# Performance work log

Measured on AMD Instinct MI355X. Metric: run time of the kernel, lower is better.

Reference implementation:

```python
import jax, jax.numpy as jnp
import numpy as np

K = 2  # num_experts_used (top-k)


def setup_inputs() -> dict:
    key = jax.random.key(0)
    ks = jax.random.split(key, 6)
    B, S, D, U, E = 2, 2048, 1024, 4096, 8
    return {
        "x": jax.random.normal(ks[0], (B, S, D), dtype=jnp.float32),
        "w_router": jax.random.normal(ks[1], (E, D), dtype=jnp.float32),
        "w_up": jax.random.normal(ks[2], (E, U, D), dtype=jnp.float32),
        "b_up": jax.random.normal(ks[3], (E, U), dtype=jnp.float32),
        "w_down": jax.random.normal(ks[4], (E, D, U), dtype=jnp.float32),
        "b_down": jax.random.normal(ks[5], (E, D), dtype=jnp.float32),
    }


def reference(x, w_router, w_up, b_up, w_down, b_down):
    # Router: Linear(embed_dim -> num_experts), no bias
    logits = jnp.einsum('bsd,ed->bse', x, w_router)
    top_logits, idx = jax.lax.top_k(logits, K)          # [b,s,k]
    router_weights = jax.nn.softmax(top_logits, axis=-1)  # softmax over top-k logits

    # Compute all-expert FFN outputs (same math as per-token gathered weights,
    # without materializing the (b,s,k,u,d) weight copies of the original).
    h = jnp.einsum('eud,bsd->bseu', w_up, x) + b_up[None, None]   # [b,s,E,u]
    h = jax.nn.gelu(h, approximate=False)
    y = jnp.einsum('edu,bseu->bsed', w_down, h) + b_down[None, None]  # [b,s,E,d]

    # Gather outputs of the top-k experts per token
    y_k = jnp.take_along_axis(y, idx[..., None], axis=2)  # [b,s,k,d]
    out = jnp.einsum('bskd,bsk->bsd', y_k, router_weights)
    return out
```

## Files before the change

kernel.cpp:

```cpp
#include <hip/hip_runtime.h>
#include <hip/hip_bf16.h>
#include <stdint.h>
#include <math.h>

#define TTOK 4096
#define DDIM 1024
#define UDIM 4096
#define NEXP 8
#define KSPLIT 2
#define KCH   (UDIM / KSPLIT)
#define NPAIR (TTOK * 2)
#define EPAD 72
#define CPAD 32
#define RBLK 128
#define CBLK 2048

using float4v = __attribute__((ext_vector_type(4))) float;
using short8  = __attribute__((ext_vector_type(8))) short;
using ushort8 = __attribute__((ext_vector_type(8))) unsigned short;
using ushort4v = __attribute__((ext_vector_type(4))) unsigned short;

__device__ __forceinline__ unsigned short f2bf(float f) {
  union { float f; unsigned u; } v; v.f = f;
  unsigned r = v.u + 0x7FFFu + ((v.u >> 16) & 1u);
  return (unsigned short)(r >> 16);
}
__device__ __forceinline__ float bf2f(unsigned short u) {
  union { unsigned u; float f; } v; v.u = ((unsigned)u) << 16;
  return v.f;
}
__device__ __forceinline__ void load_lds16(const void* g, void* l) {
  __builtin_amdgcn_global_load_lds(
      (const __attribute__((address_space(1))) unsigned int*)g,
      (__attribute__((address_space(3))) unsigned int*)l, 16, 0, 0);
}
__device__ __forceinline__ short8 cvt8(const float4v a, const float4v b) {
  union { __hip_bfloat162 h[4]; short8 s; } u;
  u.h[0] = __float22bfloat162_rn(make_float2(a[0], a[1]));
  u.h[1] = __float22bfloat162_rn(make_float2(a[2], a[3]));
  u.h[2] = __float22bfloat162_rn(make_float2(b[0], b[1]));
  u.h[3] = __float22bfloat162_rn(make_float2(b[2], b[3]));
  return u.s;
}
__device__ __forceinline__ float gelu_f(float v) {
  float u = v * (0.7978845608f + 0.0356774081f * v * v);
  float ex = __expf(2.0f * u);
  return v * (1.0f - 1.0f / (1.0f + ex));
}

__global__ void router_kernel(const float* __restrict__ x,
                              const float* __restrict__ wr,
                              int* __restrict__ counts, int* __restrict__ list,
                              float* __restrict__ wpair, int* __restrict__ epair,
                              unsigned short* __restrict__ xb) {
  const int t = blockIdx.x * 4 + (threadIdx.x >> 6);
  const int lane = threadIdx.x & 63;
  float acc[NEXP];
#pragma unroll
  for (int e = 0; e < NEXP; e++) acc[e] = 0.0f;
  const float* xr = x + (size_t)t * DDIM;
  unsigned short* xbr = xb + (size_t)t * DDIM;
  for (int d = lane; d < DDIM; d += 64) {
    float xv = xr[d];
    xbr[d] = f2bf(xv);
#pragma unroll
    for (int e = 0; e < NEXP; e++) acc[e] += xv * wr[e * DDIM + d];
  }
#pragma unroll
  for (int e = 0; e < NEXP; e++) {
#pragma unroll
    for (int off = 32; off > 0; off >>= 1) acc[e] += __shfl_xor(acc[e], off, 64);
  }
  if (lane == 0) {
    int e0 = 0; float l0 = acc[0];
    for (int e = 1; e < NEXP; e++) if (acc[e] > l0) { l0 = acc[e]; e0 = e; }
    int e1 = -1; float l1 = -3.4e38f;
    for (int e = 0; e < NEXP; e++) if (e != e0 && acc[e] > l1) { l1 = acc[e]; e1 = e; }
    float s1 = expf(l1 - l0);
    float inv = 1.0f / (1.0f + s1);
    int p0 = atomicAdd(&counts[e0 * CPAD], 1);
    list[e0 * TTOK + p0] = 2 * t;
    wpair[2 * t] = inv;  epair[2 * t] = e0;
    int p1 = atomicAdd(&counts[e1 * CPAD], 1);
    list[e1 * TTOK + p1] = 2 * t + 1;
    wpair[2 * t + 1] = s1 * inv;  epair[2 * t + 1] = e1;
  }
}

__global__ void prep_kernel(const float* __restrict__ x, const float* __restrict__ wr,
                            int* __restrict__ counts, int* __restrict__ list,
                            float* __restrict__ wpair, int* __restrict__ epair,
                            unsigned short* __restrict__ xb,
                            const float* __restrict__ wu, const float* __restrict__ wd,
                            unsigned short* __restrict__ wub, unsigned short* __restrict__ wdb) {
  __shared__ int sE0[32], sE1[32];
  const int bid = blockIdx.x;
  const int tid = threadIdx.x;

  if (bid < RBLK) {
    const int wave = tid >> 6, lane = tid & 63;
#pragma unroll 1
    for (int j = 0; j < 8; j++) {
      const int slot = wave * 8 + j;
      const int t = bid * 32 + slot;
      float acc[NEXP];
#pragma unroll
      for (int e = 0; e < NEXP; e++) acc[e] = 0.0f;
      const float* xr = x + (size_t)t * DDIM;
      unsigned short* xbr = xb + (size_t)t * DDIM;
#pragma unroll
      for (int it = 0; it < 4; it++) {
        const int d = it * 256 + lane * 4;
        float4v xv = *(const float4v*)(xr + d);
        ushort4v xo;
#pragma unroll
        for (int c = 0; c < 4; c++) xo[c] = f2bf(xv[c]);
        *(ushort4v*)(xbr + d) = xo;
#pragma unroll
        for (int e = 0; e < NEXP; e++) {
          float4v wv = *(const float4v*)(wr + e * DDIM + d);
          acc[e] += xv[0] * wv[0] + xv[1] * wv[1] + xv[2] * wv[2] + xv[3] * wv[3];
        }
      }
#pragma unroll
      for (int e = 0; e < NEXP; e++) {
#pragma unroll
        for (int off = 32; off > 0; off >>= 1) acc[e] += __shfl_xor(acc[e], off, 64);
      }
      if (lane == 0) {
        int e0 = 0; float l0 = acc[0];
        for (int e = 1; e < NEXP; e++) if (acc[e] > l0) { l0 = acc[e]; e0 = e; }
        int e1 = -1; float l1 = -3.4e38f;
        for (int e = 0; e < NEXP; e++) if (e != e0 && acc[e] > l1) { l1 = acc[e]; e1 = e; }
        float s1 = expf(l1 - l0);
        float inv = 1.0f / (1.0f + s1);
        wpair[2 * t] = inv;          epair[2 * t] = e0;
        wpair[2 * t + 1] = s1 * inv; epair[2 * t + 1] = e1;
        sE0[slot] = e0;  sE1[slot] = e1;
      }
    }
    __syncthreads();
    if (tid < NEXP) {
      const int e = tid;
      int cnt = 0;
#pragma unroll
      for (int s = 0; s < 32; s++) cnt += (sE0[s] == e) + (sE1[s] == e);
      int r = atomicAdd(&counts[e * CPAD], cnt);
      int* le = list + e * TTOK;
#pragma unroll 1
      for (int s = 0; s < 32; s++) {
        const int p = 2 * (bid * 32 + s);
        if (sE0[s] == e) le[r++] = p;
        if (sE1[s] == e) le[r++] = p + 1;
      }
    }
    return;
  }

  const int cb = bid - RBLK;
  const float* s; unsigned short* d;
  size_t i0;
  if (cb < CBLK / 2) { s = wu; d = wub; i0 = (size_t)cb * 4096; }
  else               { s = wd; d = wdb; i0 = (size_t)(cb - CBLK / 2) * 4096; }
#pragma unroll
  for (int it = 0; it < 16; it++) {
    const size_t i = i0 + (size_t)it * 256 + tid;
    float4v lo = *(const float4v*)(s + i * 8);
    float4v hi = *(const float4v*)(s + i * 8 + 4);
    *(short8*)(d + i * 8) = cvt8(lo, hi);
  }
}

__global__ __launch_bounds__(256, 4) void stage_up_b16(
    const unsigned short* __restrict__ xb, const unsigned short* __restrict__ wub,
    const float* __restrict__ bup, const int* __restrict__ counts,
    const int* __restrict__ list, unsigned short* __restrict__ h) {
  const int e = blockIdx.z, mt = blockIdx.y, nt = blockIdx.x;
  const int cnt = counts[e * CPAD];
  if (mt * 128 >= cnt) return;
  const int rem = min(128, cnt - mt * 128);
  const int* lst = list + e * TTOK + mt * 128;

  __shared__ __align__(16) char SM[18432];
  unsigned short* Sb = (unsigned short*)SM;

  const int tid = threadIdx.x;
  const int wave = tid >> 6, lane = tid & 63;
  const int srow = tid >> 2, cell = tid & 3;

  const int tok0 = lst[min(srow, rem - 1)] >> 1;
  const int tok1 = lst[min(srow + 64, rem - 1)] >> 1;
  const unsigned short* a0 = xb + (size_t)tok0 * DDIM + cell * 8;
  const unsigned short* a1 = xb + (size_t)tok1 * DDIM + cell * 8;
  const unsigned short* b0 = wub + ((size_t)e * UDIM + nt * 128 + srow) * DDIM + cell * 8;
  const unsigned short* b1 = b0 + (size_t)64 * DDIM;

  const int wm = wave >> 1, wn = wave & 1;
  const int lane15 = lane & 15, quad = lane >> 4;
  const int abyte = (wm * 64 + lane15) * 64 + quad * 16;
  const int bbyte = 8192 + (wn * 64 + lane15) * 64 + quad * 16;

  float4v acc[4][4];
#pragma unroll
  for (int i = 0; i < 4; i++)
#pragma unroll
    for (int j = 0; j < 4; j++) acc[i][j] = (float4v){0.f, 0.f, 0.f, 0.f};

  for (int k0 = 0; k0 < DDIM; k0 += 32) {
    load_lds16(a0 + k0, SM + tid * 16);
    load_lds16(a1 + k0, SM + 4096 + tid * 16);
    load_lds16(b0 + k0, SM + 8192 + tid * 16);
    load_lds16(b1 + k0, SM + 12288 + tid * 16);
    __syncthreads();
    short8 af[4], bfr[4];
#pragma unroll
    for (int mi = 0; mi < 4; mi++) af[mi] = *(const short8*)(SM + abyte + mi * 1024);
#pragma unroll
    for (int ni = 0; ni < 4; ni++) bfr[ni] = *(const short8*)(SM + bbyte + ni * 1024);
#pragma unroll
    for (int mi = 0; mi < 4; mi++)
#pragma unroll
      for (int ni = 0; ni < 4; ni++)
        acc[mi][ni] = __builtin_amdgcn_mfma_f32_16x16x32_bf16(af[mi], bfr[ni], acc[mi][ni], 0, 0, 0);
    __syncthreads();
  }

  const int ucol0 = nt * 128 + wn * 64;
  float bias[4];
#pragma unroll
  for (int ni = 0; ni < 4; ni++) bias[ni] = bup[e * UDIM + ucol0 + ni * 16 + lane15];
  const int row = tid >> 1, seg = tid & 1;
  const int opair = (row < rem) ? lst[row] : -1;
#pragma unroll
  for (int hh = 0; hh < 2; hh++) {
    if (wn == hh) {
#pragma unroll
      for (int mi = 0; mi < 4; mi++)
#pragma unroll
        for (int r = 0; r < 4; r++) {
          const int rl = wm * 64 + mi * 16 + quad * 4 + r;
#pragma unroll
          for (int ni = 0; ni < 4; ni++)
            Sb[rl * EPAD + ni * 16 + lane15] = f2bf(gelu_f(acc[mi][ni][r] + bias[ni]));
        }
    }
    __syncthreads();
    if (opair >= 0) {
      unsigned short* dst = h + (size_t)opair * UDIM + nt * 128 + hh * 64 + seg * 32;
      const unsigned short* src = Sb + row * EPAD + seg * 32;
#pragma unroll
      for (int c = 0; c < 4; c++) *(ushort8*)(dst + c * 8) = *(const ushort8*)(src + c * 8);
    }
    __syncthreads();
  }
}

__global__ __launch_bounds__(256, 4) void stage_down_b16(
    const unsigned short* __restrict__ h, const unsigned short* __restrict__ wdb,
    const int* __restrict__ counts, const int* __restrict__ list,
    unsigned short* __restrict__ part) {
  const int e = blockIdx.z, mt = blockIdx.y >> 1, kc = blockIdx.y & 1, nt = blockIdx.x;
  const int cnt = counts[e * CPAD];
  if (mt * 128 >= cnt) return;
  const int rem = min(128, cnt - mt * 128);
  const int* lst = list + e * TTOK + mt * 128;

  __shared__ __align__(16) char SM[18432];
  unsigned short* Sb = (unsigned short*)SM;

  const int tid = threadIdx.x;
  const int wave = tid >> 6, lane = tid & 63;
  const int srow = tid >> 2, cell = tid & 3;

  const int pr0 = lst[min(srow, rem - 1)];
  const int pr1 = lst[min(srow + 64, rem - 1)];
  const unsigned short* a0 = h + (size_t)pr0 * UDIM + kc * KCH + cell * 8;
  const unsigned short* a1 = h + (size_t)pr1 * UDIM + kc * KCH + cell * 8;
  const unsigned short* b0 = wdb + ((size_t)e * DDIM + nt * 128 + srow) * UDIM + kc * KCH + cell * 8;
  const unsigned short* b1 = b0 + (size_t)64 * UDIM;

  const int wm = wave >> 1, wn = wave & 1;
  const int lane15 = lane & 15, quad = lane >> 4;
  const int abyte = (wm * 64 + lane15) * 64 + quad * 16;
  const int bbyte = 8192 + (wn * 64 + lane15) * 64 + quad * 16;

  float4v acc[4][4];
#pragma unroll
  for (int i = 0; i < 4; i++)
#pragma unroll
    for (int j = 0; j < 4; j++) acc[i][j] = (float4v){0.f, 0.f, 0.f, 0.f};

  for (int k0 = 0; k0 < KCH; k0 += 32) {
    load_lds16(a0 + k0, SM + tid * 16);
    load_lds16(a1 + k0, SM + 4096 + tid * 16);
    load_lds16(b0 + k0, SM + 8192 + tid * 16);
    load_lds16(b1 + k0, SM + 12288 + tid * 16);
    __syncthreads();
    short8 af[4], bfr[4];
#pragma unroll
    for (int mi = 0; mi < 4; mi++) af[mi] = *(const short8*)(SM + abyte + mi * 1024);
#pragma unroll
    for (int ni = 0; ni < 4; ni++) bfr[ni] = *(const short8*)(SM + bbyte + ni * 1024);
#pragma unroll
    for (int mi = 0; mi < 4; mi++)
#pragma unroll
      for (int ni = 0; ni < 4; ni++)
        acc[mi][ni] = __builtin_amdgcn_mfma_f32_16x16x32_bf16(af[mi], bfr[ni], acc[mi][ni], 0, 0, 0);
    __syncthreads();
  }

  const int row = tid >> 1, seg = tid & 1;
  const int opair = (row < rem) ? lst[row] : -1;
#pragma unroll
  for (int hh = 0; hh < 2; hh++) {
    if (wn == hh) {
#pragma unroll
      for (int mi = 0; mi < 4; mi++)
#pragma unroll
        for (int r = 0; r < 4; r++) {
          const int rl = wm * 64 + mi * 16 + quad * 4 + r;
#pragma unroll
          for (int ni = 0; ni < 4; ni++)
            Sb[rl * EPAD + ni * 16 + lane15] = f2bf(acc[mi][ni][r]);
        }
    }
    __syncthreads();
    if (opair >= 0) {
      unsigned short* dst = part + ((size_t)kc * NPAIR + opair) * DDIM + nt * 128 + hh * 64 + seg * 32;
      const unsigned short* src = Sb + row * EPAD + seg * 32;
#pragma unroll
      for (int c = 0; c < 4; c++) *(ushort8*)(dst + c * 8) = *(const ushort8*)(src + c * 8);
    }
    __syncthreads();
  }
}

__global__ __launch_bounds__(256, 3) void stage_up_k(
    const unsigned short* __restrict__ xb, const float* __restrict__ wu,
    const float* __restrict__ bup, const int* __restrict__ counts,
    const int* __restrict__ list, unsigned short* __restrict__ h) {
  const int e = blockIdx.z, mt = blockIdx.y, nt = blockIdx.x;
  const int cnt = counts[e * CPAD];
  if (mt * 128 >= cnt) return;
  const int rem = min(128, cnt - mt * 128);
  const int* lst = list + e * TTOK + mt * 128;

  __shared__ __align__(16) char SM[24576];
  unsigned short* Sb = (unsigned short*)SM;

  const int tid = threadIdx.x;
  const int wave = tid >> 6, lane = tid & 63;
  const int srow = tid >> 2, cell = tid & 3;
  const int brow = tid >> 3;
  const int bswz = (tid & 7) ^ (brow & 7);

  const int tok0 = lst[min(srow, rem - 1)] >> 1;
  const int tok1 = lst[min(srow + 64, rem - 1)] >> 1;
  const unsigned short* a0 = xb + (size_t)tok0 * DDIM + cell * 8;
  const unsigned short* a1 = xb + (size_t)tok1 * DDIM + cell * 8;
  const float* bbase = wu + ((size_t)e * UDIM + nt * 128) * DDIM;
  const float* bsrc[4];
#pragma unroll
  for (int k = 0; k < 4; k++) bsrc[k] = bbase + (size_t)(brow + k * 32) * DDIM + bswz * 4;

  const int wm = wave >> 1, wn = wave & 1;
  const int lane15 = lane & 15, quad = lane >> 4;
  const int abyte = (wm * 64 + lane15) * 64 + quad * 16;
  const int p0 = (2 * quad) ^ (lane & 7);
  const int bbyte = 8192 + (wn * 64 + lane15) * 128;

  float4v acc[4][4];
#pragma unroll
  for (int i = 0; i < 4; i++)
#pragma unroll
    for (int j = 0; j < 4; j++) acc[i][j] = (float4v){0.f, 0.f, 0.f, 0.f};

  for (int k0 = 0; k0 < DDIM; k0 += 32) {
    load_lds16(a0 + k0, SM + tid * 16);
    load_lds16(a1 + k0, SM + 4096 + tid * 16);
#pragma unroll
    for (int k = 0; k < 4; k++) load_lds16(bsrc[k] + k0, SM + 8192 + k * 4096 + tid * 16);
    __syncthreads();
    short8 af[4], bfr[4];
#pragma unroll
    for (int mi = 0; mi < 4; mi++) af[mi] = *(const short8*)(SM + abyte + mi * 1024);
#pragma unroll
    for (int ni = 0; ni < 4; ni++) {
      const char* rb = SM + bbyte + ni * 2048;
      float4v f0 = *(const float4v*)(rb + p0 * 16);
      float4v f1 = *(const float4v*)(rb + (p0 ^ 1) * 16);
      bfr[ni] = cvt8(f0, f1);
    }
#pragma unroll
    for (int mi = 0; mi < 4; mi++)
#pragma unroll
      for (int ni = 0; ni < 4; ni++)
        acc[mi][ni] = __builtin_amdgcn_mfma_f32_16x16x32_bf16(af[mi], bfr[ni], acc[mi][ni], 0, 0, 0);
    __syncthreads();
  }

  const int ucol0 = nt * 128 + wn * 64;
  float bias[4];
#pragma unroll
  for (int ni = 0; ni < 4; ni++) bias[ni] = bup[e * UDIM + ucol0 + ni * 16 + lane15];
  const int row = tid >> 1, seg = tid & 1;
  const int opair = (row < rem) ? lst[row] : -1;
#pragma unroll
  for (int hh = 0; hh < 2; hh++) {
    if (wn == hh) {
#pragma unroll
      for (int mi = 0; mi < 4; mi++)
#pragma unroll
        for (int r = 0; r < 4; r++) {
          const int rl = wm * 64 + mi * 16 + quad * 4 + r;
#pragma unroll
          for (int ni = 0; ni < 4; ni++)
            Sb[rl * EPAD + ni * 16 + lane15] = f2bf(gelu_f(acc[mi][ni][r] + bias[ni]));
        }
    }
    __syncthreads();
    if (opair >= 0) {
      unsigned short* dst = h + (size_t)opair * UDIM + nt * 128 + hh * 64 + seg * 32;
      const unsigned short* src = Sb + row * EPAD + seg * 32;
#pragma unroll
      for (int c = 0; c < 4; c++) *(ushort8*)(dst + c * 8) = *(const ushort8*)(src + c * 8);
    }
    __syncthreads();
  }
}

template <bool PARTM>
__global__ __launch_bounds__(256, 3) void stage_down_k(
    const unsigned short* __restrict__ h, const float* __restrict__ wd,
    const float* __restrict__ bdn, const float* __restrict__ wpair,
    const int* __restrict__ counts, const int* __restrict__ list,
    unsigned short* __restrict__ part, float* __restrict__ out) {
  const int e = blockIdx.z, mt = blockIdx.y >> 1, kc = blockIdx.y & 1, nt = blockIdx.x;
  const int cnt = counts[e * CPAD];
  if (mt * 128 >= cnt) return;
  const int rem = min(128, cnt - mt * 128);
  const int* lst = list + e * TTOK + mt * 128;

  __shared__ __align__(16) char SM[24576];
  unsigned short* Sb = (unsigned short*)SM;

  const int tid = threadIdx.x;
  const int wave = tid >> 6, lane = tid & 63;
  const int srow = tid >> 2, cell = tid & 3;
  const int brow = tid >> 3;
  const int bswz = (tid & 7) ^ (brow & 7);

  const int pr0 = lst[min(srow, rem - 1)];
  const int pr1 = lst[min(srow + 64, rem - 1)];
  const unsigned short* a0 = h + (size_t)pr0 * UDIM + kc * KCH + cell * 8;
  const unsigned short* a1 = h + (size_t)pr1 * UDIM + kc * KCH + cell * 8;
  const float* bbase = wd + ((size_t)e * DDIM + nt * 128) * UDIM + kc * KCH;
  const float* bsrc[4];
#pragma unroll
  for (int k = 0; k < 4; k++) bsrc[k] = bbase + (size_t)(brow + k * 32) * UDIM + bswz * 4;

  const int wm = wave >> 1, wn = wave & 1;
  const int lane15 = lane & 15, quad = lane >> 4;
  const int abyte = (wm * 64 + lane15) * 64 + quad * 16;
  const int p0 = (2 * quad) ^ (lane & 7);
  const int bbyte = 8192 + (wn * 64 + lane15) * 128;

  float4v acc[4][4];
#pragma unroll
  for (int i = 0; i < 4; i++)
#pragma unroll
    for (int j = 0; j < 4; j++) acc[i][j] = (float4v){0.f, 0.f, 0.f, 0.f};

  for (int k0 = 0; k0 < KCH; k0 += 32) {
    load_lds16(a0 + k0, SM + tid * 16);
    load_lds16(a1 + k0, SM + 4096 + tid * 16);
#pragma unroll
    for (int k = 0; k < 4; k++) load_lds16(bsrc[k] + k0, SM + 8192 + k * 4096 + tid * 16);
    __syncthreads();
    short8 af[4], bfr[4];
#pragma unroll
    for (int mi = 0; mi < 4; mi++) af[mi] = *(const short8*)(SM + abyte + mi * 1024);
#pragma unroll
    for (int ni = 0; ni < 4; ni++) {
      const char* rb = SM + bbyte + ni * 2048;
      float4v f0 = *(const float4v*)(rb + p0 * 16);
      float4v f1 = *(const float4v*)(rb + (p0 ^ 1) * 16);
      bfr[ni] = cvt8(f0, f1);
    }
#pragma unroll
    for (int mi = 0; mi < 4; mi++)
#pragma unroll
      for (int ni = 0; ni < 4; ni++)
        acc[mi][ni] = __builtin_amdgcn_mfma_f32_16x16x32_bf16(af[mi], bfr[ni], acc[mi][ni], 0, 0, 0);
    __syncthreads();
  }

  const int dcol0 = nt * 128 + wn * 64;
  if constexpr (PARTM) {
    const int row = tid >> 1, seg = tid & 1;
    const int opair = (row < rem) ? lst[row] : -1;
#pragma unroll
    for (int hh = 0; hh < 2; hh++) {
      if (wn == hh) {
#pragma unroll
        for (int mi = 0; mi < 4; mi++)
#pragma unroll
          for (int r = 0; r < 4; r++) {
            const int rl = wm * 64 + mi * 16 + quad * 4 + r;
#pragma unroll
            for (int ni = 0; ni < 4; ni++)
              Sb[rl * EPAD + ni * 16 + lane15] = f2bf(acc[mi][ni][r]);
          }
      }
      __syncthreads();
      if (opair >= 0) {
        unsigned short* dst = part + ((size_t)kc * NPAIR + opair) * DDIM + nt * 128 + hh * 64 + seg * 32;
        const unsigned short* src = Sb + row * EPAD + seg * 32;
#pragma unroll
        for (int c = 0; c < 4; c++) *(ushort8*)(dst + c * 8) = *(const ushort8*)(src + c * 8);
      }
      __syncthreads();
    }
  } else {
    float bias[4];
#pragma unroll
    for (int ni = 0; ni < 4; ni++)
      bias[ni] = (kc == 0) ? bdn[e * DDIM + dcol0 + ni * 16 + lane15] : 0.0f;
#pragma unroll
    for (int mi = 0; mi < 4; mi++)
#pragma unroll
      for (int r = 0; r < 4; r++) {
        const int mrow = wm * 64 + mi * 16 + quad * 4 + r;
        if (mrow < rem) {
          const int pair = lst[mrow];
          const float w = wpair[pair];
          float* orow = out + (size_t)(pair >> 1) * DDIM;
#pragma unroll
          for (int ni = 0; ni < 4; ni++)
            atomicAdd(&orow[dcol0 + ni * 16 + lane15], w * (acc[mi][ni][r] + bias[ni]));
        }
      }
  }
}

__global__ void combine_kernel(const unsigned short* __restrict__ part,
                               const float* __restrict__ bdn,
                               const float* __restrict__ wpair,
                               const int* __restrict__ epair,
                               float* __restrict__ out) {
  const int idx = blockIdx.x * 256 + threadIdx.x;
  const int t = idx >> 7, c8 = (idx & 127) * 8;
  const size_t kstride = (size_t)NPAIR * DDIM;
  const unsigned short* pa = part + (size_t)(2 * t) * DDIM + c8;
  float s0[8], s1[8];
#pragma unroll
  for (int j = 0; j < 8; j++) { s0[j] = 0.f; s1[j] = 0.f; }
#pragma unroll
  for (int kc = 0; kc < KSPLIT; kc++) {
    ushort8 a = *(const ushort8*)(pa + kc * kstride);
    ushort8 b = *(const ushort8*)(pa + kc * kstride + DDIM);
#pragma unroll
    for (int j = 0; j < 8; j++) { s0[j] += bf2f(a[j]); s1[j] += bf2f(b[j]); }
  }
  const float w0 = wpair[2 * t], w1 = wpair[2 * t + 1];
  const int e0 = epair[2 * t], e1 = epair[2 * t + 1];
  const float* b0 = bdn + e0 * DDIM + c8;
  const float* b1 = bdn + e1 * DDIM + c8;
  float4v o[2];
#pragma unroll
  for (int half = 0; half < 2; half++)
#pragma unroll
    for (int j = 0; j < 4; j++) {
      const int jj = half * 4 + j;
      o[half][j] = w0 * (s0[jj] + b0[jj]) + w1 * (s1[jj] + b1[jj]);
    }
  float4v* dst = (float4v*)(out + (size_t)t * DDIM + c8);
  dst[0] = o[0]; dst[1] = o[1];
}

__global__ void zero_out_k(float4v* __restrict__ out) {
  const int tid = blockIdx.x * blockDim.x + threadIdx.x;
  const int O4 = TTOK * DDIM / 4;
  const int stride = gridDim.x * blockDim.x;
  for (int i = tid; i < O4; i += stride) out[i] = (float4v){0.f, 0.f, 0.f, 0.f};
}

extern "C" void kernel_launch(void* const* d_in, const int* in_sizes, int n_in,
                              void* d_out, int out_size, void* d_ws, size_t ws_size,
                              hipStream_t stream) {
  (void)in_sizes; (void)n_in; (void)out_size;
  const float* x        = (const float*)d_in[0];
  const float* w_router = (const float*)d_in[1];
  const float* w_up     = (const float*)d_in[2];
  const float* b_up     = (const float*)d_in[3];
  const float* w_down   = (const float*)d_in[4];
  const float* b_down   = (const float*)d_in[5];
  float* out = (float*)d_out;

  char* ws = (char*)d_ws;
  size_t off = 0;
  auto take = [&](size_t b) { size_t o = off; off = (off + b + 255) & ~(size_t)255; return o; };
  unsigned short* h  = (unsigned short*)(ws + take((size_t)NPAIR * UDIM * 2));
  unsigned short* xb = (unsigned short*)(ws + take((size_t)TTOK * DDIM * 2));
  int* counts        = (int*)(ws + take(NEXP * CPAD * 4));
  int* list          = (int*)(ws + take((size_t)NEXP * TTOK * 4));
  float* wpair       = (float*)(ws + take((size_t)NPAIR * 4));
  int* epair         = (int*)(ws + take((size_t)NPAIR * 4));
  size_t part_off    = take((size_t)KSPLIT * NPAIR * DDIM * 2);
  const bool partmode = ws_size >= off;
  size_t wub_off     = take((size_t)NEXP * UDIM * DDIM * 2);
  size_t wdb_off     = take((size_t)NEXP * DDIM * UDIM * 2);
  const bool bf16mode = ws_size >= off;

  hipMemsetAsync(counts, 0, NEXP * CPAD * 4, stream);

  if (bf16mode) {
    unsigned short* part = (unsigned short*)(ws + part_off);
    unsigned short* wub  = (unsigned short*)(ws + wub_off);
    unsigned short* wdb  = (unsigned short*)(ws + wdb_off);
    prep_kernel<<<RBLK + CBLK, 256, 0, stream>>>(
        x, w_router, counts, list, wpair, epair, xb, w_up, w_down, wub, wdb);
    stage_up_b16<<<dim3(UDIM / 128, 32, NEXP), 256, 0, stream>>>(
        xb, wub, b_up, counts, list, h);
    stage_down_b16<<<dim3(DDIM / 128, 32 * KSPLIT, NEXP), 256, 0, stream>>>(
        h, wdb, counts, list, part);
    combine_kernel<<<TTOK * DDIM / 8 / 256, 256, 0, stream>>>(part, b_down, wpair, epair, out);
  } else {
    router_kernel<<<TTOK / 4, 256, 0, stream>>>(x, w_router, counts, list, wpair, epair, xb);
    stage_up_k<<<dim3(UDIM / 128, 32, NEXP), 256, 0, stream>>>(xb, w_up, b_up, counts, list, h);
    if (partmode) {
      unsigned short* part = (unsigned short*)(ws + part_off);
      stage_down_k<true><<<dim3(DDIM / 128, 32 * KSPLIT, NEXP), 256, 0, stream>>>(
          h, w_down, b_down, wpair, counts, list, part, out);
      combine_kernel<<<TTOK * DDIM / 8 / 256, 256, 0, stream>>>(part, b_down, wpair, epair, out);
    } else {
      zero_out_k<<<1024, 256, 0, stream>>>((float4v*)out);
      stage_down_k<false><<<dim3(DDIM / 128, 32 * KSPLIT, NEXP), 256, 0, stream>>>(
          h, w_down, b_down, wpair, counts, list, (unsigned short*)nullptr, out);
    }
  }
}
```

Measured before the change: 602.9 us.

## Reorder prep blocks, use nontemporal weight conversion, expert-major grids, rework fallback path

```diff
diff --git a/kernel.cpp b/kernel.cpp
--- a/kernel.cpp
+++ b/kernel.cpp
@@ -14,6 +14,7 @@
 #define CPAD 32
 #define RBLK 128
 #define CBLK 2048
+#define RTOK 16
 
 using float4v = __attribute__((ext_vector_type(4))) float;
 using short8  = __attribute__((ext_vector_type(8))) short;
@@ -33,6 +34,12 @@
   __builtin_amdgcn_global_load_lds(
       (const __attribute__((address_space(1))) unsigned int*)g,
       (__attribute__((address_space(3))) unsigned int*)l, 16, 0, 0);
+}
+__device__ __forceinline__ float4v ntld4(const float* p) {
+  return __builtin_nontemporal_load((const float4v*)p);
+}
+__device__ __forceinline__ void ntst8(unsigned short* p, const short8 v) {
+  __builtin_nontemporal_store(v, (short8*)p);
 }
 __device__ __forceinline__ short8 cvt8(const float4v a, const float4v b) {
   union { __hip_bfloat162 h[4]; short8 s; } u;
@@ -46,45 +53,6 @@
   float u = v * (0.7978845608f + 0.0356774081f * v * v);
   float ex = __expf(2.0f * u);
   return v * (1.0f - 1.0f / (1.0f + ex));
-}
-
-__global__ void router_kernel(const float* __restrict__ x,
-                              const float* __restrict__ wr,
-                              int* __restrict__ counts, int* __restrict__ list,
-                              float* __restrict__ wpair, int* __restrict__ epair,
-                              unsigned short* __restrict__ xb) {
-  const int t = blockIdx.x * 4 + (threadIdx.x >> 6);
-  const int lane = threadIdx.x & 63;
-  float acc[NEXP];
-#pragma unroll
-  for (int e = 0; e < NEXP; e++) acc[e] = 0.0f;
-  const float* xr = x + (size_t)t * DDIM;
-  unsigned short* xbr = xb + (size_t)t * DDIM;
-  for (int d = lane; d < DDIM; d += 64) {
-    float xv = xr[d];
-    xbr[d] = f2bf(xv);
-#pragma unroll
-    for (int e = 0; e < NEXP; e++) acc[e] += xv * wr[e * DDIM + d];
-  }
-#pragma unroll
-  for (int e = 0; e < NEXP; e++) {
-#pragma unroll
-    for (int off = 32; off > 0; off >>= 1) acc[e] += __shfl_xor(acc[e], off, 64);
-  }
-  if (lane == 0) {
-    int e0 = 0; float l0 = acc[0];
-    for (int e = 1; e < NEXP; e++) if (acc[e] > l0) { l0 = acc[e]; e0 = e; }
-    int e1 = -1; float l1 = -3.4e38f;
-    for (int e = 0; e < NEXP; e++) if (e != e0 && acc[e] > l1) { l1 = acc[e]; e1 = e; }
-    float s1 = expf(l1 - l0);
-    float inv = 1.0f / (1.0f + s1);
-    int p0 = atomicAdd(&counts[e0 * CPAD], 1);
-    list[e0 * TTOK + p0] = 2 * t;
-    wpair[2 * t] = inv;  epair[2 * t] = e0;
-    int p1 = atomicAdd(&counts[e1 * CPAD], 1);
-    list[e1 * TTOK + p1] = 2 * t + 1;
-    wpair[2 * t + 1] = s1 * inv;  epair[2 * t + 1] = e1;
-  }
 }
 
 __global__ void prep_kernel(const float* __restrict__ x, const float* __restrict__ wr,
@@ -97,77 +65,81 @@
   const int bid = blockIdx.x;
   const int tid = threadIdx.x;
 
-  if (bid < RBLK) {
-    const int wave = tid >> 6, lane = tid & 63;
+  if (bid < CBLK) {
+    const float* s; unsigned short* d; size_t i0;
+    if (bid < CBLK / 2) { s = wu; d = wub; i0 = (size_t)bid * 4096; }
+    else                { s = wd; d = wdb; i0 = (size_t)(bid - CBLK / 2) * 4096; }
+    const float* sp = s + (i0 + tid) * 8;
+    unsigned short* dp = d + (i0 + tid) * 8;
+    float4v p0 = ntld4(sp), p1 = ntld4(sp + 4);
+#pragma unroll
+    for (int it = 0; it < 16; it++) {
+      float4v c0 = p0, c1 = p1;
+      if (it + 1 < 16) {
+        p0 = ntld4(sp + (size_t)(it + 1) * 2048);
+        p1 = ntld4(sp + (size_t)(it + 1) * 2048 + 4);
+      }
+      ntst8(dp + (size_t)it * 2048, cvt8(c0, c1));
+    }
+    return;
+  }
+
+  const int rb = bid - CBLK;
+  const int wave = tid >> 6, lane = tid & 63;
 #pragma unroll 1
-    for (int j = 0; j < 8; j++) {
-      const int slot = wave * 8 + j;
-      const int t = bid * 32 + slot;
-      float acc[NEXP];
-#pragma unroll
-      for (int e = 0; e < NEXP; e++) acc[e] = 0.0f;
-      const float* xr = x + (size_t)t * DDIM;
-      unsigned short* xbr = xb + (size_t)t * DDIM;
-#pragma unroll
-      for (int it = 0; it < 4; it++) {
-        const int d = it * 256 + lane * 4;
-        float4v xv = *(const float4v*)(xr + d);
-        ushort4v xo;
-#pragma unroll
-        for (int c = 0; c < 4; c++) xo[c] = f2bf(xv[c]);
-        *(ushort4v*)(xbr + d) = xo;
-#pragma unroll
-        for (int e = 0; e < NEXP; e++) {
-          float4v wv = *(const float4v*)(wr + e * DDIM + d);
-          acc[e] += xv[0] * wv[0] + xv[1] * wv[1] + xv[2] * wv[2] + xv[3] * wv[3];
-        }
+  for (int j = 0; j < 8; j++) {
+    const int slot = wave * 8 + j;
+    const int t = rb * 32 + slot;
+    float acc[NEXP];
+#pragma unroll
+    for (int e = 0; e < NEXP; e++) acc[e] = 0.0f;
+    const float* xr = x + (size_t)t * DDIM;
+    unsigned short* xbr = xb + (size_t)t * DDIM;
+#pragma unroll
+    for (int it = 0; it < 4; it++) {
+      const int d = it * 256 + lane * 4;
+      float4v xv = *(const float4v*)(xr + d);
+      ushort4v xo;
+#pragma unroll
+      for (int c = 0; c < 4; c++) xo[c] = f2bf(xv[c]);
+      *(ushort4v*)(xbr + d) = xo;
+#pragma unroll
+      for (int e = 0; e < NEXP; e++) {
+        float4v wv = *(const float4v*)(wr + e * DDIM + d);
+        acc[e] += xv[0] * wv[0] + xv[1] * wv[1] + xv[2] * wv[2] + xv[3] * wv[3];
       }
-#pragma unroll
-      for (int e = 0; e < NEXP; e++) {
-#pragma unroll
-        for (int off = 32; off > 0; off >>= 1) acc[e] += __shfl_xor(acc[e], off, 64);
-      }
-      if (lane == 0) {
-        int e0 = 0; float l0 = acc[0];
-        for (int e = 1; e < NEXP; e++) if (acc[e] > l0) { l0 = acc[e]; e0 = e; }
-        int e1 = -1; float l1 = -3.4e38f;
-        for (int e = 0; e < NEXP; e++) if (e != e0 && acc[e] > l1) { l1 = acc[e]; e1 = e; }
-        float s1 = expf(l1 - l0);
-        float inv = 1.0f / (1.0f + s1);
-        wpair[2 * t] = inv;          epair[2 * t] = e0;
-        wpair[2 * t + 1] = s1 * inv; epair[2 * t + 1] = e1;
-        sE0[slot] = e0;  sE1[slot] = e1;
-      }
-    }
-    __syncthreads();
-    if (tid < NEXP) {
-      const int e = tid;
-      int cnt = 0;
-#pragma unroll
-      for (int s = 0; s < 32; s++) cnt += (sE0[s] == e) + (sE1[s] == e);
-      int r = atomicAdd(&counts[e * CPAD], cnt);
-      int* le = list + e * TTOK;
+    }
+#pragma unroll
+    for (int e = 0; e < NEXP; e++) {
+#pragma unroll
+      for (int off = 32; off > 0; off >>= 1) acc[e] += __shfl_xor(acc[e], off, 64);
+    }
+    if (lane == 0) {
+      int e0 = 0; float l0 = acc[0];
+      for (int e = 1; e < NEXP; e++) if (acc[e] > l0) { l0 = acc[e]; e0 = e; }
+      int e1 = -1; float l1 = -3.4e38f;
+      for (int e = 0; e < NEXP; e++) if (e != e0 && acc[e] > l1) { l1 = acc[e]; e1 = e; }
+      float s1 = expf(l1 - l0);
+      float inv = 1.0f / (1.0f + s1);
+      wpair[2 * t] = inv;          epair[2 * t] = e0;
+      wpair[2 * t + 1] = s1 * inv; epair[2 * t + 1] = e1;
+      sE0[slot] = e0;  sE1[slot] = e1;
+    }
+  }
+  __syncthreads();
+  if (tid < NEXP) {
+    const int e = tid;
+    int cnt = 0;
+#pragma unroll
+    for (int s = 0; s < 32; s++) cnt += (sE0[s] == e) + (sE1[s] == e);
+    int r = atomicAdd(&counts[e * CPAD], cnt);
+    int* le = list + e * TTOK;
 #pragma unroll 1
-      for (int s = 0; s < 32; s++) {
-        const int p = 2 * (bid * 32 + s);
-        if (sE0[s] == e) le[r++] = p;
-        if (sE1[s] == e) le[r++] = p + 1;
-      }
-    }
-    return;
-  }
-
-  const int cb = bid - RBLK;
-  const float* s; unsigned short* d;
-  size_t i0;
-  if (cb < CBLK / 2) { s = wu; d = wub; i0 = (size_t)cb * 4096; }
-  else               { s = wd; d = wdb; i0 = (size_t)(cb - CBLK / 2) * 4096; }
-#pragma unroll
-  for (int it = 0; it < 16; it++) {
-    const size_t i = i0 + (size_t)it * 256 + tid;
-    float4v lo = *(const float4v*)(s + i * 8);
-    float4v hi = *(const float4v*)(s + i * 8 + 4);
-    *(short8*)(d + i * 8) = cvt8(lo, hi);
+    for (int s = 0; s < 32; s++) {
+      const int p = 2 * (rb * 32 + s);
+      if (sE0[s] == e) le[r++] = p;
+      if (sE1[s] == e) le[r++] = p + 1;
+    }
   }
 }
 
@@ -175,7 +147,7 @@
     const unsigned short* __restrict__ xb, const unsigned short* __restrict__ wub,
     const float* __restrict__ bup, const int* __restrict__ counts,
     const int* __restrict__ list, unsigned short* __restrict__ h) {
-  const int e = blockIdx.z, mt = blockIdx.y, nt = blockIdx.x;
+  const int e = blockIdx.x, nt = blockIdx.y, mt = blockIdx.z;
   const int cnt = counts[e * CPAD];
   if (mt * 128 >= cnt) return;
   const int rem = min(128, cnt - mt * 128);
@@ -259,7 +231,7 @@
     const unsigned short* __restrict__ h, const unsigned short* __restrict__ wdb,
     const int* __restrict__ counts, const int* __restrict__ list,
     unsigned short* __restrict__ part) {
-  const int e = blockIdx.z, mt = blockIdx.y >> 1, kc = blockIdx.y & 1, nt = blockIdx.x;
+  const int e = blockIdx.x, nt = blockIdx.y, mt = blockIdx.z >> 1, kc = blockIdx.z & 1;
   const int cnt = counts[e * CPAD];
   if (mt * 128 >= cnt) return;
   const int rem = min(128, cnt - mt * 128);
@@ -335,7 +307,73 @@
   }
 }
 
-__global__ __launch_bounds__(256, 3) void stage_up_k(
+__global__ void router_kernel(const float* __restrict__ x,
+                              const float* __restrict__ wr,
+                              int* __restrict__ counts, int* __restrict__ list,
+                              float* __restrict__ wpair, int* __restrict__ epair,
+                              unsigned short* __restrict__ xb) {
+  __shared__ int sE0[RTOK], sE1[RTOK];
+  const int bid = blockIdx.x;
+  const int tid = threadIdx.x;
+  const int wave = tid >> 6, lane = tid & 63;
+#pragma unroll 1
+  for (int j = 0; j < RTOK / 4; j++) {
+    const int slot = wave * (RTOK / 4) + j;
+    const int t = bid * RTOK + slot;
+    float acc[NEXP];
+#pragma unroll
+    for (int e = 0; e < NEXP; e++) acc[e] = 0.0f;
+    const float* xr = x + (size_t)t * DDIM;
+    unsigned short* xbr = xb + (size_t)t * DDIM;
+#pragma unroll
+    for (int it = 0; it < 4; it++) {
+      const int d = it * 256 + lane * 4;
+      float4v xv = *(const float4v*)(xr + d);
+      ushort4v xo;
+#pragma unroll
+      for (int c = 0; c < 4; c++) xo[c] = f2bf(xv[c]);
+      *(ushort4v*)(xbr + d) = xo;
+#pragma unroll
+      for (int e = 0; e < NEXP; e++) {
+        float4v wv = *(const float4v*)(wr + e * DDIM + d);
+        acc[e] += xv[0] * wv[0] + xv[1] * wv[1] + xv[2] * wv[2] + xv[3] * wv[3];
+      }
+    }
+#pragma unroll
+    for (int e = 0; e < NEXP; e++) {
+#pragma unroll
+      for (int off = 32; off > 0; off >>= 1) acc[e] += __shfl_xor(acc[e], off, 64);
+    }
+    if (lane == 0) {
+      int e0 = 0; float l0 = acc[0];
+      for (int e = 1; e < NEXP; e++) if (acc[e] > l0) { l0 = acc[e]; e0 = e; }
+      int e1 = -1; float l1 = -3.4e38f;
+      for (int e = 0; e < NEXP; e++) if (e != e0 && acc[e] > l1) { l1 = acc[e]; e1 = e; }
+      float s1 = expf(l1 - l0);
+      float inv = 1.0f / (1.0f + s1);
+      wpair[2 * t] = inv;          epair[2 * t] = e0;
+      wpair[2 * t + 1] = s1 * inv; epair[2 * t + 1] = e1;
+      sE0[slot] = e0;  sE1[slot] = e1;
+    }
+  }
+  __syncthreads();
+  if (tid < NEXP) {
+    const int e = tid;
+    int cnt = 0;
+#pragma unroll
+    for (int s = 0; s < RTOK; s++) cnt += (sE0[s] == e) + (sE1[s] == e);
+    int r = atomicAdd(&counts[e * CPAD], cnt);
+    int* le = list + e * TTOK;
+#pragma unroll 1
+    for (int s = 0; s < RTOK; s++) {
+      const int p = 2 * (bid * RTOK + s);
+      if (sE0[s] == e) le[r++] = p;
+      if (sE1[s] == e) le[r++] = p + 1;
+    }
+  }
+}
+
+__global__ __launch_bounds__(256, 4) void stage_up_rs(
     const unsigned short* __restrict__ xb, const float* __restrict__ wu,
     const float* __restrict__ bup, const int* __restrict__ counts,
     const int* __restrict__ list, unsigned short* __restrict__ h) {
@@ -345,29 +383,29 @@
   const int rem = min(128, cnt - mt * 128);
   const int* lst = list + e * TTOK + mt * 128;
 
-  __shared__ __align__(16) char SM[24576];
+  __shared__ __align__(16) char SM[18432];
   unsigned short* Sb = (unsigned short*)SM;
 
   const int tid = threadIdx.x;
   const int wave = tid >> 6, lane = tid & 63;
   const int srow = tid >> 2, cell = tid & 3;
-  const int brow = tid >> 3;
-  const int bswz = (tid & 7) ^ (brow & 7);
 
   const int tok0 = lst[min(srow, rem - 1)] >> 1;
   const int tok1 = lst[min(srow + 64, rem - 1)] >> 1;
   const unsigned short* a0 = xb + (size_t)tok0 * DDIM + cell * 8;
   const unsigned short* a1 = xb + (size_t)tok1 * DDIM + cell * 8;
-  const float* bbase = wu + ((size_t)e * UDIM + nt * 128) * DDIM;
-  const float* bsrc[4];
-#pragma unroll
-  for (int k = 0; k < 4; k++) bsrc[k] = bbase + (size_t)(brow + k * 32) * DDIM + bswz * 4;
+  const float* bw0 = wu + ((size_t)e * UDIM + nt * 128 + srow) * DDIM + cell * 8;
+  const float* bw1 = bw0 + (size_t)64 * DDIM;
 
   const int wm = wave >> 1, wn = wave & 1;
   const int lane15 = lane & 15, quad = lane >> 4;
   const int abyte = (wm * 64 + lane15) * 64 + quad * 16;
-  const int p0 = (2 * quad) ^ (lane & 7);
-  const int bbyte = 8192 + (wn * 64 + lane15) * 128;
+  const int bbyte = 8192 + (wn * 64 + lane15) * 64 + quad * 16;
+
+  float4v p00 = *(const float4v*)(bw0);
+  float4v p01 = *(const float4v*)(bw0 + 4);
+  float4v p10 = *(const float4v*)(bw1);
+  float4v p11 = *(const float4v*)(bw1 + 4);
 
   float4v acc[4][4];
 #pragma unroll
@@ -378,19 +416,22 @@
   for (int k0 = 0; k0 < DDIM; k0 += 32) {
     load_lds16(a0 + k0, SM + tid * 16);
     load_lds16(a1 + k0, SM + 4096 + tid * 16);
-#pragma unroll
-    for (int k = 0; k < 4; k++) load_lds16(bsrc[k] + k0, SM + 8192 + k * 4096 + tid * 16);
+    short8 bv0 = cvt8(p00, p01);
+    short8 bv1 = cvt8(p10, p11);
+    if (k0 + 32 < DDIM) {
+      p00 = *(const float4v*)(bw0 + k0 + 32);
+      p01 = *(const float4v*)(bw0 + k0 + 36);
+      p10 = *(const float4v*)(bw1 + k0 + 32);
+      p11 = *(const float4v*)(bw1 + k0 + 36);
+    }
+    *(short8*)(SM + 8192 + tid * 16) = bv0;
+    *(short8*)(SM + 12288 + tid * 16) = bv1;
     __syncthreads();
     short8 af[4], bfr[4];
 #pragma unroll
     for (int mi = 0; mi < 4; mi++) af[mi] = *(const short8*)(SM + abyte + mi * 1024);
 #pragma unroll
-    for (int ni = 0; ni < 4; ni++) {
-      const char* rb = SM + bbyte + ni * 2048;
-      float4v f0 = *(const float4v*)(rb + p0 * 16);
-      float4v f1 = *(const float4v*)(rb + (p0 ^ 1) * 16);
-      bfr[ni] = cvt8(f0, f1);
-    }
+    for (int ni = 0; ni < 4; ni++) bfr[ni] = *(const short8*)(SM + bbyte + ni * 1024);
 #pragma unroll
     for (int mi = 0; mi < 4; mi++)
 #pragma unroll
@@ -429,41 +470,39 @@
   }
 }
 
-template <bool PARTM>
-__global__ __launch_bounds__(256, 3) void stage_down_k(
+__global__ __launch_bounds__(256, 4) void stage_down_rs(
     const unsigned short* __restrict__ h, const float* __restrict__ wd,
-    const float* __restrict__ bdn, const float* __restrict__ wpair,
     const int* __restrict__ counts, const int* __restrict__ list,
-    unsigned short* __restrict__ part, float* __restrict__ out) {
-  const int e = blockIdx.z, mt = blockIdx.y >> 1, kc = blockIdx.y & 1, nt = blockIdx.x;
+    unsigned short* __restrict__ part) {
+  const int e = blockIdx.z, mt = blockIdx.x >> 1, kc = blockIdx.x & 1, nt = blockIdx.y;
   const int cnt = counts[e * CPAD];
   if (mt * 128 >= cnt) return;
   const int rem = min(128, cnt - mt * 128);
   const int* lst = list + e * TTOK + mt * 128;
 
-  __shared__ __align__(16) char SM[24576];
+  __shared__ __align__(16) char SM[18432];
   unsigned short* Sb = (unsigned short*)SM;
 
   const int tid = threadIdx.x;
   const int wave = tid >> 6, lane = tid & 63;
   const int srow = tid >> 2, cell = tid & 3;
-  const int brow = tid >> 3;
-  const int bswz = (tid & 7) ^ (brow & 7);
 
   const int pr0 = lst[min(srow, rem - 1)];
   const int pr1 = lst[min(srow + 64, rem - 1)];
   const unsigned short* a0 = h + (size_t)pr0 * UDIM + kc * KCH + cell * 8;
   const unsigned short* a1 = h + (size_t)pr1 * UDIM + kc * KCH + cell * 8;
-  const float* bbase = wd + ((size_t)e * DDIM + nt * 128) * UDIM + kc * KCH;
-  const float* bsrc[4];
-#pragma unroll
-  for (int k = 0; k < 4; k++) bsrc[k] = bbase + (size_t)(brow + k * 32) * UDIM + bswz * 4;
+  const float* bw0 = wd + ((size_t)e * DDIM + nt * 128 + srow) * UDIM + kc * KCH + cell * 8;
+  const float* bw1 = bw0 + (size_t)64 * UDIM;
 
   const int wm = wave >> 1, wn = wave & 1;
   const int lane15 = lane & 15, quad = lane >> 4;
   const int abyte = (wm * 64 + lane15) * 64 + quad * 16;
-  const int p0 = (2 * quad) ^ (lane & 7);
-  const int bbyte = 8192 + (wn * 64 + lane15) * 128;
+  const int bbyte = 8192 + (wn * 64 + lane15) * 64 + quad * 16;
+
+  float4v p00 = *(const float4v*)(bw0);
+  float4v p01 = *(const float4v*)(bw0 + 4);
+  float4v p10 = *(const float4v*)(bw1);
+  float4v p11 = *(const float4v*)(bw1 + 4);
 
   float4v acc[4][4];
 #pragma unroll
@@ -474,19 +513,22 @@
   for (int k0 = 0; k0 < KCH; k0 += 32) {
     load_lds16(a0 + k0, SM + tid * 16);
     load_lds16(a1 + k0, SM + 4096 + tid * 16);
-#pragma unroll
-    for (int k = 0; k < 4; k++) load_lds16(bsrc[k] + k0, SM + 8192 + k * 4096 + tid * 16);
+    short8 bv0 = cvt8(p00, p01);
+    short8 bv1 = cvt8(p10, p11);
+    if (k0 + 32 < KCH) {
+      p00 = *(const float4v*)(bw0 + k0 + 32);
+      p01 = *(const float4v*)(bw0 + k0 + 36);
+      p10 = *(const float4v*)(bw1 + k0 + 32);
+      p11 = *(const float4v*)(bw1 + k0 + 36);
+    }
+    *(short8*)(SM + 8192 + tid * 16) = bv0;
+    *(short8*)(SM + 12288 + tid * 16) = bv1;
     __syncthreads();
     short8 af[4], bfr[4];
 #pragma unroll
     for (int mi = 0; mi < 4; mi++) af[mi] = *(const short8*)(SM + abyte + mi * 1024);
 #pragma unroll
-    for (int ni = 0; ni < 4; ni++) {
-      const char* rb = SM + bbyte + ni * 2048;
-      float4v f0 = *(const float4v*)(rb + p0 * 16);
-      float4v f1 = *(const float4v*)(rb + (p0 ^ 1) * 16);
-      bfr[ni] = cvt8(f0, f1);
-    }
+    for (int ni = 0; ni < 4; ni++) bfr[ni] = *(const short8*)(SM + bbyte + ni * 1024);
 #pragma unroll
     for (int mi = 0; mi < 4; mi++)
 #pragma unroll
@@ -495,51 +537,29 @@
     __syncthreads();
   }
 
-  const int dcol0 = nt * 128 + wn * 64;
-  if constexpr (PARTM) {
-    const int row = tid >> 1, seg = tid & 1;
-    const int opair = (row < rem) ? lst[row] : -1;
-#pragma unroll
-    for (int hh = 0; hh < 2; hh++) {
-      if (wn == hh) {
-#pragma unroll
-        for (int mi = 0; mi < 4; mi++)
-#pragma unroll
-          for (int r = 0; r < 4; r++) {
-            const int rl = wm * 64 + mi * 16 + quad * 4 + r;
-#pragma unroll
-            for (int ni = 0; ni < 4; ni++)
-              Sb[rl * EPAD + ni * 16 + lane15] = f2bf(acc[mi][ni][r]);
-          }
-      }
-      __syncthreads();
-      if (opair >= 0) {
-        unsigned short* dst = part + ((size_t)kc * NPAIR + opair) * DDIM + nt * 128 + hh * 64 + seg * 32;
-        const unsigned short* src = Sb + row * EPAD + seg * 32;
-#pragma unroll
-        for (int c = 0; c < 4; c++) *(ushort8*)(dst + c * 8) = *(const ushort8*)(src + c * 8);
-      }
-      __syncthreads();
-    }
-  } else {
-    float bias[4];
-#pragma unroll
-    for (int ni = 0; ni < 4; ni++)
-      bias[ni] = (kc == 0) ? bdn[e * DDIM + dcol0 + ni * 16 + lane15] : 0.0f;
-#pragma unroll
-    for (int mi = 0; mi < 4; mi++)
-#pragma unroll
-      for (int r = 0; r < 4; r++) {
-        const int mrow = wm * 64 + mi * 16 + quad * 4 + r;
-        if (mrow < rem) {
-          const int pair = lst[mrow];
-          const float w = wpair[pair];
-          float* orow = out + (size_t)(pair >> 1) * DDIM;
+  const int row = tid >> 1, seg = tid & 1;
+  const int opair = (row < rem) ? lst[row] : -1;
+#pragma unroll
+  for (int hh = 0; hh < 2; hh++) {
+    if (wn == hh) {
+#pragma unroll
+      for (int mi = 0; mi < 4; mi++)
+#pragma unroll
+        for (int r = 0; r < 4; r++) {
+          const int rl = wm * 64 + mi * 16 + quad * 4 + r;
 #pragma unroll
           for (int ni = 0; ni < 4; ni++)
-            atomicAdd(&orow[dcol0 + ni * 16 + lane15], w * (acc[mi][ni][r] + bias[ni]));
+            Sb[rl * EPAD + ni * 16 + lane15] = f2bf(acc[mi][ni][r]);
         }
-      }
+    }
+    __syncthreads();
+    if (opair >= 0) {
+      unsigned short* dst = part + ((size_t)kc * NPAIR + opair) * DDIM + nt * 128 + hh * 64 + seg * 32;
+      const unsigned short* src = Sb + row * EPAD + seg * 32;
+#pragma unroll
+      for (int c = 0; c < 4; c++) *(ushort8*)(dst + c * 8) = *(const ushort8*)(src + c * 8);
+    }
+    __syncthreads();
   }
 }
 
@@ -576,13 +596,6 @@
     }
   float4v* dst = (float4v*)(out + (size_t)t * DDIM + c8);
   dst[0] = o[0]; dst[1] = o[1];
-}
-
-__global__ void zero_out_k(float4v* __restrict__ out) {
-  const int tid = blockIdx.x * blockDim.x + threadIdx.x;
-  const int O4 = TTOK * DDIM / 4;
-  const int stride = gridDim.x * blockDim.x;
-  for (int i = tid; i < O4; i += stride) out[i] = (float4v){0.f, 0.f, 0.f, 0.f};
 }
 
 extern "C" void kernel_launch(void* const* d_in, const int* in_sizes, int n_in,
@@ -607,6 +620,7 @@
   float* wpair       = (float*)(ws + take((size_t)NPAIR * 4));
   int* epair         = (int*)(ws + take((size_t)NPAIR * 4));
   size_t part_off    = take((size_t)KSPLIT * NPAIR * DDIM * 2);
+  unsigned short* part = (unsigned short*)(ws + part_off);
   const bool partmode = ws_size >= off;
   size_t wub_off     = take((size_t)NEXP * UDIM * DDIM * 2);
   size_t wdb_off     = take((size_t)NEXP * DDIM * UDIM * 2);
@@ -615,28 +629,20 @@
   hipMemsetAsync(counts, 0, NEXP * CPAD * 4, stream);
 
   if (bf16mode) {
-    unsigned short* part = (unsigned short*)(ws + part_off);
-    unsigned short* wub  = (unsigned short*)(ws + wub_off);
-    unsigned short* wdb  = (unsigned short*)(ws + wdb_off);
-    prep_kernel<<<RBLK + CBLK, 256, 0, stream>>>(
+    unsigned short* wub = (unsigned short*)(ws + wub_off);
+    unsigned short* wdb = (unsigned short*)(ws + wdb_off);
+    prep_kernel<<<CBLK + RBLK, 256, 0, stream>>>(
         x, w_router, counts, list, wpair, epair, xb, w_up, w_down, wub, wdb);
-    stage_up_b16<<<dim3(UDIM / 128, 32, NEXP), 256, 0, stream>>>(
+    stage_up_b16<<<dim3(NEXP, UDIM / 128, 32), 256, 0, stream>>>(
         xb, wub, b_up, counts, list, h);
-    stage_down_b16<<<dim3(DDIM / 128, 32 * KSPLIT, NEXP), 256, 0, stream>>>(
+    stage_down_b16<<<dim3(NEXP, DDIM / 128, 32 * KSPLIT), 256, 0, stream>>>(
         h, wdb, counts, list, part);
     combine_kernel<<<TTOK * DDIM / 8 / 256, 256, 0, stream>>>(part, b_down, wpair, epair, out);
-  } else {
-    router_kernel<<<TTOK / 4, 256, 0, stream>>>(x, w_router, counts, list, wpair, epair, xb);
-    stage_up_k<<<dim3(UDIM / 128, 32, NEXP), 256, 0, stream>>>(xb, w_up, b_up, counts, list, h);
-    if (partmode) {
-      unsigned short* part = (unsigned short*)(ws + part_off);
-      stage_down_k<true><<<dim3(DDIM / 128, 32 * KSPLIT, NEXP), 256, 0, stream>>>(
-          h, w_down, b_down, wpair, counts, list, part, out);
-      combine_kernel<<<TTOK * DDIM / 8 / 256, 256, 0, stream>>>(part, b_down, wpair, epair, out);
-    } else {
-      zero_out_k<<<1024, 256, 0, stream>>>((float4v*)out);
-      stage_down_k<false><<<dim3(DDIM / 128, 32 * KSPLIT, NEXP), 256, 0, stream>>>(
-          h, w_down, b_down, wpair, counts, list, (unsigned short*)nullptr, out);
-    }
-  }
-}
+  } else if (partmode) {
+    router_kernel<<<TTOK / RTOK, 256, 0, stream>>>(x, w_router, counts, list, wpair, epair, xb);
+    stage_up_rs<<<dim3(UDIM / 128, 32, NEXP), 256, 0, stream>>>(xb, w_up, b_up, counts, list, h);
+    stage_down_rs<<<dim3(32 * KSPLIT, DDIM / 128, NEXP), 256, 0, stream>>>(
+        h, w_down, counts, list, part);
+    combine_kernel<<<TTOK * DDIM / 8 / 256, 256, 0, stream>>>(part, b_down, wpair, epair, out);
+  }
+}
```

Measured after the change: 571.1 us. 5.3% less time.
